# Optimization experiments

Measured on AMD Instinct MI355X. Metric: run time of the kernel, lower is better.

The kernel has to match this reference:

```python
import jax, jax.numpy as jnp
import numpy as np

N = 500          # max_neurons, all alive
INPUT_SIZE = 3072
FEAT_DIM = 64
OUT_SIZE = 10
BATCH = 8192
RADIUS = 20.0
VOL = 100.0      # cubic volume (100,100,100)
N_ITER = 3


def setup_inputs() -> dict:
    key = jax.random.key(0)
    k_x, k_pos, k_iw, k_f, k_ow = jax.random.split(key, 5)
    x = jax.random.normal(k_x, (BATCH, INPUT_SIZE), dtype=jnp.float32)
    # seed positions spread across the volume, roughly matching _init_seeds
    positions = jax.random.uniform(k_pos, (N, 3), dtype=jnp.float32) * 80.0 + 10.0
    input_weights = jax.random.normal(k_iw, (N, INPUT_SIZE), dtype=jnp.float32) * 0.02
    features = jax.random.normal(k_f, (N, FEAT_DIM), dtype=jnp.float32) * 0.1
    output_weights = jax.random.normal(k_ow, (N, OUT_SIZE), dtype=jnp.float32) * 0.02
    biases = jnp.zeros((N,), dtype=jnp.float32)
    return {"x": x, "positions": positions, "input_weights": input_weights,
            "features": features, "output_weights": output_weights, "biases": biases}


def reference(x, positions, input_weights, features, output_weights, biases):
    # clamp positions into the volume (per-axis, vol is cubic here)
    pos = jnp.clip(positions, 0.1, VOL - 0.1)  # [N,3]

    # pairwise distances (grad-safe sqrt at the zero diagonal)
    diff = pos[:, None, :] - pos[None, :, :]          # [N,N,3]
    sq = jnp.sum(diff * diff, axis=-1)                # [N,N]
    pos_mask = sq > 0.0
    dist = jnp.where(pos_mask, jnp.sqrt(jnp.where(pos_mask, sq, 1.0)), 0.0)

    conn_mask = (dist < RADIUS) & (dist > 0.0)
    attenuation = jnp.exp(-dist / RADIUS) * conn_mask.astype(dist.dtype)

    # feature similarity (F.normalize clamps the norm from below at eps)
    feat_norm = features / jnp.maximum(
        jnp.linalg.norm(features, axis=1, keepdims=True), 1e-6)
    feat_sim = jnp.clip(feat_norm @ feat_norm.T, -1.0, 1.0)  # [N,N]

    conn_w = attenuation * (0.5 + 0.5 * feat_sim)
    conn_w = conn_w / (jnp.sum(conn_w, axis=1, keepdims=True) + 1e-6)

    # input gating: neurons near x=0 receive input
    x_norm = pos[:, 0] / VOL                          # [N]
    input_weight = jnp.exp(-2.0 * x_norm)
    input_weight = input_weight / (jnp.sum(input_weight) + 1e-6)

    activations = x @ input_weights.T * input_weight + biases  # [B,N]

    # iterative message passing (fixed small iteration count)
    for _ in range(N_ITER):
        msg = activations @ conn_w.T                  # [B,N]
        activations = jnp.minimum(jax.nn.relu(activations + 0.5 * msg), 50.0)

    # output gating: neurons near x=VOL emit output
    output_weight = jnp.exp(2.0 * (x_norm - 1.0))
    output_weight = output_weight / (jnp.sum(output_weight) + 1e-6)

    return activations @ (output_weights * output_weight[:, None])  # [B,OUT]
```

## Files before the change

### kernel.cpp

```cpp
#include <hip/hip_runtime.h>
#include <stdint.h>

#define N_REAL 500
#define NPAD   512
#define K_IN   3072
#define NBATCH 8192
#define NOUT   10
#define RADIUS 20.0f
#define VOLF   100.0f

typedef __attribute__((ext_vector_type(8))) __bf16 bf16x8;
typedef __attribute__((ext_vector_type(4))) float  f32x4;
typedef __attribute__((ext_vector_type(4))) unsigned short us4;

__device__ __forceinline__ unsigned short f2bf(float f) {
    unsigned int u = __float_as_uint(f);
    u += 0x7FFFu + ((u >> 16) & 1u);
    return (unsigned short)(u >> 16);
}
__device__ __forceinline__ float bf2f(unsigned short h) {
    return __uint_as_float(((unsigned int)h) << 16);
}
__device__ __forceinline__ uint2 cvt_pk4(float4 v) {
    uint2 r;
    asm("v_cvt_pk_bf16_f32 %0, %1, %2" : "=v"(r.x) : "v"(v.x), "v"(v.y));
    asm("v_cvt_pk_bf16_f32 %0, %1, %2" : "=v"(r.y) : "v"(v.z), "v"(v.w));
    return r;
}

#define GLOBAL_AS __attribute__((address_space(1)))
#define LDS_AS    __attribute__((address_space(3)))
__device__ __forceinline__ void glds16(const void* g, void* l) {
    __builtin_amdgcn_global_load_lds((const GLOBAL_AS void*)g, (LDS_AS void*)l, 16, 0, 0);
}

__global__ void prep1(const float* __restrict__ positions,
                      const float* __restrict__ features,
                      const float* __restrict__ out_w,
                      const float* __restrict__ biases,
                      float* __restrict__ feat_norm,
                      float* __restrict__ pos_c,
                      float* __restrict__ inw,
                      float* __restrict__ biasp,
                      float* __restrict__ wout)
{
    int n = threadIdx.x;
    float e_in = 0.f, e_out = 0.f;
    float px = 0.f, py = 0.f, pz = 0.f;
    if (n < N_REAL) {
        px = fminf(fmaxf(positions[n*3+0], 0.1f), VOLF - 0.1f);
        py = fminf(fmaxf(positions[n*3+1], 0.1f), VOLF - 0.1f);
        pz = fminf(fmaxf(positions[n*3+2], 0.1f), VOLF - 0.1f);
        float xn = px / VOLF;
        e_in  = expf(-2.f * xn);
        e_out = expf(2.f * (xn - 1.f));
        float ss = 0.f;
        for (int f = 0; f < 64; ++f) { float v = features[n*64+f]; ss += v*v; }
        float nm = fmaxf(sqrtf(ss), 1e-6f);
        for (int f = 0; f < 64; ++f) feat_norm[n*64+f] = features[n*64+f] / nm;
    } else {
        for (int f = 0; f < 64; ++f) feat_norm[n*64+f] = 0.f;
    }
    pos_c[n*4+0] = px; pos_c[n*4+1] = py; pos_c[n*4+2] = pz; pos_c[n*4+3] = 0.f;

    __shared__ float s_in[512], s_out[512];
    s_in[n] = e_in; s_out[n] = e_out;
    __syncthreads();
    for (int s = 256; s > 0; s >>= 1) {
        if (n < s) { s_in[n] += s_in[n+s]; s_out[n] += s_out[n+s]; }
        __syncthreads();
    }
    float sum_in  = s_in[0]  + 1e-6f;
    float sum_out = s_out[0] + 1e-6f;

    inw[n]   = (n < N_REAL) ? (e_in / sum_in) : 0.f;
    biasp[n] = (n < N_REAL) ? biases[n] : 0.f;
    float wo = (n < N_REAL) ? (e_out / sum_out) : 0.f;
    for (int o = 0; o < NOUT; ++o)
        wout[n*NOUT + o] = (n < N_REAL) ? out_w[n*NOUT + o] * wo : 0.f;
}

__global__ void prep2(const float* __restrict__ pos_c,
                      const float* __restrict__ feat_norm,
                      unsigned short* __restrict__ conn_w)
{
    int i = blockIdx.x;
    int t = threadIdx.x;
    __shared__ float fi[64];
    __shared__ float spos[4];
    __shared__ float red[128];
    if (t < 64) fi[t] = feat_norm[i*64 + t];
    if (t < 4)  spos[t] = pos_c[i*4 + t];
    __syncthreads();

    float w[4];
    float part = 0.f;
    for (int jj = 0; jj < 4; ++jj) {
        int j = t + jj*128;
        float val = 0.f;
        if (i < N_REAL && j < N_REAL) {
            float dx = spos[0] - pos_c[j*4+0];
            float dy = spos[1] - pos_c[j*4+1];
            float dz = spos[2] - pos_c[j*4+2];
            float sq = dx*dx + dy*dy + dz*dz;
            if (sq > 0.f) {
                float dist = sqrtf(sq);
                if (dist < RADIUS) {
                    float att = expf(-dist / RADIUS);
                    float sim = 0.f;
                    const float4* fj = (const float4*)(feat_norm + j*64);
                    const float4* fi4 = (const float4*)fi;
                    #pragma unroll
                    for (int f = 0; f < 16; ++f) {
                        float4 a = fi4[f]; float4 b = fj[f];
                        sim += a.x*b.x + a.y*b.y + a.z*b.z + a.w*b.w;
                    }
                    sim = fminf(fmaxf(sim, -1.f), 1.f);
                    val = att * (0.5f + 0.5f*sim);
                }
            }
        }
        w[jj] = val; part += val;
    }
    red[t] = part;
    __syncthreads();
    for (int s = 64; s > 0; s >>= 1) {
        if (t < s) red[t] += red[t+s];
        __syncthreads();
    }
    float inv = 1.f / (red[0] + 1e-6f);
    for (int jj = 0; jj < 4; ++jj)
        conn_w[(long)i*NPAD + t + jj*128] = f2bf(w[jj] * inv);
}

__global__ void cast_pad(const float* __restrict__ src, unsigned short* __restrict__ dst,
                         long total_q, long src_q)
{
    long i = (long)blockIdx.x * blockDim.x + threadIdx.x;
    long stride = (long)gridDim.x * blockDim.x;
    for (; i < total_q; i += stride) {
        us4 o;
        if (i < src_q) {
            float4 v = ((const float4*)src)[i];
            o[0] = f2bf(v.x); o[1] = f2bf(v.y); o[2] = f2bf(v.z); o[3] = f2bf(v.w);
        } else {
            o[0] = 0; o[1] = 0; o[2] = 0; o[3] = 0;
        }
        ((us4*)dst)[i] = o;
    }
}

__device__ __forceinline__ void block_map(int b, int& m0, int& n0) {
    int xcd = b & 7, loc = b >> 3;
    m0 = (xcd*16 + (loc >> 3)) * 64;
    n0 = (loc & 7) * 64;
}

__global__ __launch_bounds__(256)
void gemm1(const float* __restrict__ X,
           const unsigned short* __restrict__ B,
           unsigned short* __restrict__ Cbf,
           const float* __restrict__ inw,
           const float* __restrict__ biasp)
{
    __shared__ unsigned short As[64*64];
    __shared__ unsigned short Bs[64*64];

    const int tid  = threadIdx.x;
    const int lane = tid & 63;
    const int wave = tid >> 6;
    int m0, n0; block_map(blockIdx.x, m0, n0);
    const int wm = (wave >> 1) * 32;
    const int wn = (wave & 1) * 32;

    f32x4 acc[2][2];
    #pragma unroll
    for (int i = 0; i < 2; ++i)
        #pragma unroll
        for (int j = 0; j < 2; ++j)
            acc[i][j] = (f32x4){0.f,0.f,0.f,0.f};

    const float4* gA[4]; int lAo[4];
    #pragma unroll
    for (int s = 0; s < 4; ++s) {
        int f = tid + s*256;
        int row = f >> 4, c4 = f & 15;
        gA[s] = (const float4*)(X + (long)(m0 + row) * K_IN) + c4;
        lAo[s] = row*128 + ((c4*8) ^ ((row & 7) << 4));
    }
    const char* gB[2]; char* lB[2];
    #pragma unroll
    for (int s = 0; s < 2; ++s) {
        int o = tid*16 + s*4096;
        int row = o >> 7, d = o & 127;
        gB[s] = (const char*)B + (long)(n0 + row) * (K_IN*2) + (d ^ ((row & 7) << 4));
        lB[s] = (char*)Bs + o;
    }

    for (int t = 0; t < 48; ++t) {
        __syncthreads();
        glds16(gB[0], lB[0]);
        glds16(gB[1], lB[1]);
        gB[0] += 128; gB[1] += 128;
        float4 v[4];
        #pragma unroll
        for (int s = 0; s < 4; ++s) { v[s] = gA[s][0]; gA[s] += 16; }
        #pragma unroll
        for (int s = 0; s < 4; ++s)
            *(uint2*)((char*)As + lAo[s]) = cvt_pk4(v[s]);
        asm volatile("s_waitcnt vmcnt(0) lgkmcnt(0)" ::: "memory");
        __syncthreads();

        #pragma unroll
        for (int kk = 0; kk < 2; ++kk) {
            const int cb = kk*64 + (lane >> 4) * 16;
            bf16x8 afr[2], bfr[2];
            #pragma unroll
            for (int i = 0; i < 2; ++i) {
                int r = wm + i*16 + (lane & 15);
                afr[i] = *(const bf16x8*)((const char*)As + r*128 + (cb ^ ((r & 7) << 4)));
            }
            #pragma unroll
            for (int j = 0; j < 2; ++j) {
                int r = wn + j*16 + (lane & 15);
                bfr[j] = *(const bf16x8*)((const char*)Bs + r*128 + (cb ^ ((r & 7) << 4)));
            }
            #pragma unroll
            for (int i = 0; i < 2; ++i)
                #pragma unroll
                for (int j = 0; j < 2; ++j)
                    acc[i][j] = __builtin_amdgcn_mfma_f32_16x16x32_bf16(afr[i], bfr[j], acc[i][j], 0, 0, 0);
        }
    }

    const int mbase = m0 + wm + (lane >> 4) * 4;
    const int nbase = n0 + wn + (lane & 15);
    #pragma unroll
    for (int j = 0; j < 2; ++j) {
        const int n = nbase + j*16;
        const float win = inw[n], bia = biasp[n];
        #pragma unroll
        for (int i = 0; i < 2; ++i)
            #pragma unroll
            for (int r = 0; r < 4; ++r) {
                const long m = mbase + i*16 + r;
                Cbf[m*NPAD + n] = f2bf(acc[i][j][r] * win + bia);
            }
    }
}

__global__ __launch_bounds__(256)
void gemm2(const unsigned short* __restrict__ A,
           const unsigned short* __restrict__ B,
           unsigned short* __restrict__ Cbf,
           const unsigned short* __restrict__ actOld)
{
    __shared__ unsigned short As[64*64];
    __shared__ unsigned short Bs[64*64];

    const int tid  = threadIdx.x;
    const int lane = tid & 63;
    const int wave = tid >> 6;
    int m0, n0; block_map(blockIdx.x, m0, n0);
    const int wm = (wave >> 1) * 32;
    const int wn = (wave & 1) * 32;

    f32x4 acc[2][2];
    #pragma unroll
    for (int i = 0; i < 2; ++i)
        #pragma unroll
        for (int j = 0; j < 2; ++j)
            acc[i][j] = (f32x4){0.f,0.f,0.f,0.f};

    const char* gA[2]; char* lA[2];
    #pragma unroll
    for (int s = 0; s < 2; ++s) {
        int o = tid*16 + s*4096;
        int row = o >> 7, d = o & 127;
        gA[s] = (const char*)A + (long)(m0 + row) * (NPAD*2) + (d ^ ((row & 7) << 4));
        lA[s] = (char*)As + o;
    }
    const char* gB[2]; char* lB[2];
    #pragma unroll
    for (int s = 0; s < 2; ++s) {
        int o = tid*16 + s*4096;
        int row = o >> 7, d = o & 127;
        gB[s] = (const char*)B + (long)(n0 + row) * (NPAD*2) + (d ^ ((row & 7) << 4));
        lB[s] = (char*)Bs + o;
    }

    const int mbase = m0 + wm + (lane >> 4) * 4;
    const int nbase = n0 + wn + (lane & 15);
    unsigned short oldv[2][8];
    #pragma unroll
    for (int j = 0; j < 2; ++j)
        #pragma unroll
        for (int i = 0; i < 2; ++i)
            #pragma unroll
            for (int r = 0; r < 4; ++r)
                oldv[j][i*4+r] = actOld[(long)(mbase + i*16 + r)*NPAD + nbase + j*16];

    for (int t = 0; t < 8; ++t) {
        __syncthreads();
        #pragma unroll
        for (int s = 0; s < 2; ++s) { glds16(gA[s], lA[s]); gA[s] += 128; }
        #pragma unroll
        for (int s = 0; s < 2; ++s) { glds16(gB[s], lB[s]); gB[s] += 128; }
        asm volatile("s_waitcnt vmcnt(0)" ::: "memory");
        __syncthreads();

        #pragma unroll
        for (int kk = 0; kk < 2; ++kk) {
            const int cb = kk*64 + (lane >> 4) * 16;
            bf16x8 afr[2], bfr[2];
            #pragma unroll
            for (int i = 0; i < 2; ++i) {
                int r = wm + i*16 + (lane & 15);
                afr[i] = *(const bf16x8*)((const char*)As + r*128 + (cb ^ ((r & 7) << 4)));
            }
            #pragma unroll
            for (int j = 0; j < 2; ++j) {
                int r = wn + j*16 + (lane & 15);
                bfr[j] = *(const bf16x8*)((const char*)Bs + r*128 + (cb ^ ((r & 7) << 4)));
            }
            #pragma unroll
            for (int i = 0; i < 2; ++i)
                #pragma unroll
                for (int j = 0; j < 2; ++j)
                    acc[i][j] = __builtin_amdgcn_mfma_f32_16x16x32_bf16(afr[i], bfr[j], acc[i][j], 0, 0, 0);
        }
    }

    #pragma unroll
    for (int j = 0; j < 2; ++j) {
        const int n = nbase + j*16;
        #pragma unroll
        for (int i = 0; i < 2; ++i)
            #pragma unroll
            for (int r = 0; r < 4; ++r) {
                const long m = mbase + i*16 + r;
                float old = bf2f(oldv[j][i*4+r]);
                float vv = fminf(fmaxf(old + 0.5f * acc[i][j][r], 0.f), 50.f);
                Cbf[m*NPAD + n] = f2bf(vv);
            }
    }
}

__global__ __launch_bounds__(256)
void out_gemm(const unsigned short* __restrict__ act,
              const float* __restrict__ wout,
              float* __restrict__ out)
{
    __shared__ float sw[NPAD * NOUT];
    const int tid = threadIdx.x;
    for (int i = tid; i < NPAD*NOUT; i += 256) sw[i] = wout[i];
    __syncthreads();

    const int lane = tid & 63;
    const int wv   = tid >> 6;
    const int row  = blockIdx.x * 4 + wv;

    const unsigned short* ap = act + (long)row * NPAD + lane * 8;
    us4 v0 = *(const us4*)(ap);
    us4 v1 = *(const us4*)(ap + 4);

    float p[NOUT];
    #pragma unroll
    for (int o = 0; o < NOUT; ++o) p[o] = 0.f;

    const int nb = lane * 8;
    #pragma unroll
    for (int e = 0; e < 8; ++e) {
        float a = bf2f(e < 4 ? v0[e] : v1[e-4]);
        const float* wr = &sw[(nb + e) * NOUT];
        #pragma unroll
        for (int o = 0; o < NOUT; ++o) p[o] += a * wr[o];
    }
    #pragma unroll
    for (int o = 0; o < NOUT; ++o) {
        float s = p[o];
        for (int d = 32; d > 0; d >>= 1) s += __shfl_down(s, d);
        if (lane == 0) out[(long)row * NOUT + o] = s;
    }
}

extern "C" void kernel_launch(void* const* d_in, const int* in_sizes, int n_in,
                              void* d_out, int out_size, void* d_ws, size_t ws_size,
                              hipStream_t stream)
{
    const float* x        = (const float*)d_in[0];
    const float* pos      = (const float*)d_in[1];
    const float* in_w     = (const float*)d_in[2];
    const float* feats    = (const float*)d_in[3];
    const float* out_w    = (const float*)d_in[4];
    const float* biases   = (const float*)d_in[5];
    float* out = (float*)d_out;

    char* ws = (char*)d_ws;
    unsigned short* iw_bf  = (unsigned short*)(ws);
    unsigned short* connw  = (unsigned short*)(ws + 3145728);
    unsigned short* act_a  = (unsigned short*)(ws + 3670016);
    unsigned short* act_b  = (unsigned short*)(ws + 12058624);
    float* feat_norm = (float*)(ws + 20447232);
    float* pos_c     = (float*)(ws + 20578304);
    float* inw       = (float*)(ws + 20586496);
    float* biasp     = (float*)(ws + 20588544);
    float* wout      = (float*)(ws + 20590592);

    prep1<<<1, 512, 0, stream>>>(pos, feats, out_w, biases, feat_norm, pos_c, inw, biasp, wout);
    prep2<<<512, 128, 0, stream>>>(pos_c, feat_norm, connw);
    cast_pad<<<512, 256, 0, stream>>>(in_w, iw_bf, 393216L, 384000L);

    gemm1<<<1024, 256, 0, stream>>>(x, iw_bf, act_a, inw, biasp);
    gemm2<<<1024, 256, 0, stream>>>(act_a, connw, act_b, act_a);
    gemm2<<<1024, 256, 0, stream>>>(act_b, connw, act_a, act_b);
    gemm2<<<1024, 256, 0, stream>>>(act_a, connw, act_b, act_a);

    out_gemm<<<NBATCH/4, 256, 0, stream>>>(act_b, wout, out);
}
```

Before: 127.2 us.

## Double-buffer LDS tiles in gemm1 and gemm2 to overlap loads with MFMA

```diff
diff --git a/kernel.cpp b/kernel.cpp
--- a/kernel.cpp
+++ b/kernel.cpp
@@ -163,8 +163,8 @@
            const float* __restrict__ inw,
            const float* __restrict__ biasp)
 {
-    __shared__ unsigned short As[64*64];
-    __shared__ unsigned short Bs[64*64];
+    __shared__ unsigned short As[2][64*64];
+    __shared__ unsigned short Bs[2][64*64];
 
     const int tid  = threadIdx.x;
     const int lane = tid & 63;
@@ -188,28 +188,42 @@
         gA[s] = (const float4*)(X + (long)(m0 + row) * K_IN) + c4;
         lAo[s] = row*128 + ((c4*8) ^ ((row & 7) << 4));
     }
-    const char* gB[2]; char* lB[2];
+    const char* gB[2]; int lBo[2];
     #pragma unroll
     for (int s = 0; s < 2; ++s) {
         int o = tid*16 + s*4096;
         int row = o >> 7, d = o & 127;
         gB[s] = (const char*)B + (long)(n0 + row) * (K_IN*2) + (d ^ ((row & 7) << 4));
-        lB[s] = (char*)Bs + o;
-    }
+        lBo[s] = o;
+    }
+
+    float4 v[4];
+    #pragma unroll
+    for (int s = 0; s < 4; ++s) { v[s] = gA[s][0]; gA[s] += 16; }
+    __builtin_amdgcn_sched_barrier(0);
+    glds16(gB[0], (char*)Bs[0] + lBo[0]);
+    glds16(gB[1], (char*)Bs[0] + lBo[1]);
+    gB[0] += 128; gB[1] += 128;
+    #pragma unroll
+    for (int s = 0; s < 4; ++s)
+        *(uint2*)((char*)As[0] + lAo[s]) = cvt_pk4(v[s]);
+    asm volatile("s_waitcnt lgkmcnt(0)" ::: "memory");
 
     for (int t = 0; t < 48; ++t) {
-        __syncthreads();
-        glds16(gB[0], lB[0]);
-        glds16(gB[1], lB[1]);
-        gB[0] += 128; gB[1] += 128;
-        float4 v[4];
-        #pragma unroll
-        for (int s = 0; s < 4; ++s) { v[s] = gA[s][0]; gA[s] += 16; }
-        #pragma unroll
-        for (int s = 0; s < 4; ++s)
-            *(uint2*)((char*)As + lAo[s]) = cvt_pk4(v[s]);
-        asm volatile("s_waitcnt vmcnt(0) lgkmcnt(0)" ::: "memory");
-        __syncthreads();
+        const int cur = t & 1;
+        const bool more = (t < 47);
+        if (more) {
+            #pragma unroll
+            for (int s = 0; s < 4; ++s) { v[s] = gA[s][0]; gA[s] += 16; }
+            __builtin_amdgcn_sched_barrier(0);
+            glds16(gB[0], (char*)Bs[cur^1] + lBo[0]);
+            glds16(gB[1], (char*)Bs[cur^1] + lBo[1]);
+            gB[0] += 128; gB[1] += 128;
+            asm volatile("s_waitcnt vmcnt(6)" ::: "memory");
+        } else {
+            asm volatile("s_waitcnt vmcnt(0)" ::: "memory");
+        }
+        __builtin_amdgcn_s_barrier();
 
         #pragma unroll
         for (int kk = 0; kk < 2; ++kk) {
@@ -218,18 +232,26 @@
             #pragma unroll
             for (int i = 0; i < 2; ++i) {
                 int r = wm + i*16 + (lane & 15);
-                afr[i] = *(const bf16x8*)((const char*)As + r*128 + (cb ^ ((r & 7) << 4)));
+                afr[i] = *(const bf16x8*)((const char*)As[cur] + r*128 + (cb ^ ((r & 7) << 4)));
             }
             #pragma unroll
             for (int j = 0; j < 2; ++j) {
                 int r = wn + j*16 + (lane & 15);
-                bfr[j] = *(const bf16x8*)((const char*)Bs + r*128 + (cb ^ ((r & 7) << 4)));
+                bfr[j] = *(const bf16x8*)((const char*)Bs[cur] + r*128 + (cb ^ ((r & 7) << 4)));
             }
             #pragma unroll
             for (int i = 0; i < 2; ++i)
                 #pragma unroll
                 for (int j = 0; j < 2; ++j)
                     acc[i][j] = __builtin_amdgcn_mfma_f32_16x16x32_bf16(afr[i], bfr[j], acc[i][j], 0, 0, 0);
+        }
+
+        if (more) {
+            #pragma unroll
+            for (int s = 0; s < 4; ++s)
+                *(uint2*)((char*)As[cur^1] + lAo[s]) = cvt_pk4(v[s]);
+            asm volatile("s_waitcnt lgkmcnt(0)" ::: "memory");
+            __builtin_amdgcn_s_barrier();
         }
     }
 
@@ -255,8 +277,8 @@
            unsigned short* __restrict__ Cbf,
            const unsigned short* __restrict__ actOld)
 {
-    __shared__ unsigned short As[64*64];
-    __shared__ unsigned short Bs[64*64];
+    __shared__ unsigned short As[2][64*64];
+    __shared__ unsigned short Bs[2][64*64];
 
     const int tid  = threadIdx.x;
     const int lane = tid & 63;
@@ -272,42 +294,41 @@
         for (int j = 0; j < 2; ++j)
             acc[i][j] = (f32x4){0.f,0.f,0.f,0.f};
 
-    const char* gA[2]; char* lA[2];
+    const char* gA[2]; int lAo[2];
     #pragma unroll
     for (int s = 0; s < 2; ++s) {
         int o = tid*16 + s*4096;
         int row = o >> 7, d = o & 127;
         gA[s] = (const char*)A + (long)(m0 + row) * (NPAD*2) + (d ^ ((row & 7) << 4));
-        lA[s] = (char*)As + o;
-    }
-    const char* gB[2]; char* lB[2];
+        lAo[s] = o;
+    }
+    const char* gB[2]; int lBo[2];
     #pragma unroll
     for (int s = 0; s < 2; ++s) {
         int o = tid*16 + s*4096;
         int row = o >> 7, d = o & 127;
         gB[s] = (const char*)B + (long)(n0 + row) * (NPAD*2) + (d ^ ((row & 7) << 4));
-        lB[s] = (char*)Bs + o;
-    }
-
-    const int mbase = m0 + wm + (lane >> 4) * 4;
-    const int nbase = n0 + wn + (lane & 15);
-    unsigned short oldv[2][8];
-    #pragma unroll
-    for (int j = 0; j < 2; ++j)
-        #pragma unroll
-        for (int i = 0; i < 2; ++i)
-            #pragma unroll
-            for (int r = 0; r < 4; ++r)
-                oldv[j][i*4+r] = actOld[(long)(mbase + i*16 + r)*NPAD + nbase + j*16];
+        lBo[s] = o;
+    }
+
+    #pragma unroll
+    for (int s = 0; s < 2; ++s) { glds16(gA[s], (char*)As[0] + lAo[s]); gA[s] += 128; }
+    #pragma unroll
+    for (int s = 0; s < 2; ++s) { glds16(gB[s], (char*)Bs[0] + lBo[s]); gB[s] += 128; }
 
     for (int t = 0; t < 8; ++t) {
-        __syncthreads();
-        #pragma unroll
-        for (int s = 0; s < 2; ++s) { glds16(gA[s], lA[s]); gA[s] += 128; }
-        #pragma unroll
-        for (int s = 0; s < 2; ++s) { glds16(gB[s], lB[s]); gB[s] += 128; }
-        asm volatile("s_waitcnt vmcnt(0)" ::: "memory");
-        __syncthreads();
+        const int cur = t & 1;
+        const bool more = (t < 7);
+        if (more) {
+            #pragma unroll
+            for (int s = 0; s < 2; ++s) { glds16(gA[s], (char*)As[cur^1] + lAo[s]); gA[s] += 128; }
+            #pragma unroll
+            for (int s = 0; s < 2; ++s) { glds16(gB[s], (char*)Bs[cur^1] + lBo[s]); gB[s] += 128; }
+            asm volatile("s_waitcnt vmcnt(4)" ::: "memory");
+        } else {
+            asm volatile("s_waitcnt vmcnt(0)" ::: "memory");
+        }
+        __builtin_amdgcn_s_barrier();
 
         #pragma unroll
         for (int kk = 0; kk < 2; ++kk) {
@@ -316,12 +337,12 @@
             #pragma unroll
             for (int i = 0; i < 2; ++i) {
                 int r = wm + i*16 + (lane & 15);
-                afr[i] = *(const bf16x8*)((const char*)As + r*128 + (cb ^ ((r & 7) << 4)));
+                afr[i] = *(const bf16x8*)((const char*)As[cur] + r*128 + (cb ^ ((r & 7) << 4)));
             }
             #pragma unroll
             for (int j = 0; j < 2; ++j) {
                 int r = wn + j*16 + (lane & 15);
-                bfr[j] = *(const bf16x8*)((const char*)Bs + r*128 + (cb ^ ((r & 7) << 4)));
+                bfr[j] = *(const bf16x8*)((const char*)Bs[cur] + r*128 + (cb ^ ((r & 7) << 4)));
             }
             #pragma unroll
             for (int i = 0; i < 2; ++i)
@@ -329,8 +350,13 @@
                 for (int j = 0; j < 2; ++j)
                     acc[i][j] = __builtin_amdgcn_mfma_f32_16x16x32_bf16(afr[i], bfr[j], acc[i][j], 0, 0, 0);
         }
-    }
-
+
+        if (more)
+            __builtin_amdgcn_s_barrier();
+    }
+
+    const int mbase = m0 + wm + (lane >> 4) * 4;
+    const int nbase = n0 + wn + (lane & 15);
     #pragma unroll
     for (int j = 0; j < 2; ++j) {
         const int n = nbase + j*16;
@@ -339,7 +365,7 @@
             #pragma unroll
             for (int r = 0; r < 4; ++r) {
                 const long m = mbase + i*16 + r;
-                float old = bf2f(oldv[j][i*4+r]);
+                float old = bf2f(actOld[m*NPAD + n]);
                 float vv = fminf(fmaxf(old + 0.5f * acc[i][j][r], 0.f), 50.f);
                 Cbf[m*NPAD + n] = f2bf(vv);
             }
```

Result: slower. 130.8 us (+2.8%).

## Split-K the input GEMM and triple-buffer the message-passing GEMM with wider tiles

Applied to the files above, without the earlier changes.

```diff
diff --git a/kernel.cpp b/kernel.cpp
--- a/kernel.cpp
+++ b/kernel.cpp
@@ -150,18 +150,21 @@
     }
 }
 
-__device__ __forceinline__ void block_map(int b, int& m0, int& n0) {
+__device__ __forceinline__ void block_map_g1(int b, int& m0, int& n0) {
     int xcd = b & 7, loc = b >> 3;
     m0 = (xcd*16 + (loc >> 3)) * 64;
     n0 = (loc & 7) * 64;
 }
+__device__ __forceinline__ void block_map_g2(int b, int& m0, int& n0) {
+    int xcd = b & 7, loc = b >> 3;
+    m0 = (xcd*16 + (loc >> 2)) * 64;
+    n0 = (loc & 3) * 128;
+}
 
 __global__ __launch_bounds__(256)
-void gemm1(const float* __restrict__ X,
-           const unsigned short* __restrict__ B,
-           unsigned short* __restrict__ Cbf,
-           const float* __restrict__ inw,
-           const float* __restrict__ biasp)
+void gemm1s(const float* __restrict__ X,
+            const unsigned short* __restrict__ B,
+            float* __restrict__ Pf)
 {
     __shared__ unsigned short As[64*64];
     __shared__ unsigned short Bs[64*64];
@@ -169,7 +172,10 @@
     const int tid  = threadIdx.x;
     const int lane = tid & 63;
     const int wave = tid >> 6;
-    int m0, n0; block_map(blockIdx.x, m0, n0);
+    const int bs   = blockIdx.x & 1023;
+    const int ks   = blockIdx.x >> 10;
+    const int kbase = ks * (K_IN/2);
+    int m0, n0; block_map_g1(bs, m0, n0);
     const int wm = (wave >> 1) * 32;
     const int wn = (wave & 1) * 32;
 
@@ -185,7 +191,7 @@
     for (int s = 0; s < 4; ++s) {
         int f = tid + s*256;
         int row = f >> 4, c4 = f & 15;
-        gA[s] = (const float4*)(X + (long)(m0 + row) * K_IN) + c4;
+        gA[s] = (const float4*)(X + (long)(m0 + row) * K_IN + kbase) + c4;
         lAo[s] = row*128 + ((c4*8) ^ ((row & 7) << 4));
     }
     const char* gB[2]; char* lB[2];
@@ -193,11 +199,11 @@
     for (int s = 0; s < 2; ++s) {
         int o = tid*16 + s*4096;
         int row = o >> 7, d = o & 127;
-        gB[s] = (const char*)B + (long)(n0 + row) * (K_IN*2) + (d ^ ((row & 7) << 4));
+        gB[s] = (const char*)B + (long)(n0 + row) * (K_IN*2) + kbase*2 + (d ^ ((row & 7) << 4));
         lB[s] = (char*)Bs + o;
     }
 
-    for (int t = 0; t < 48; ++t) {
+    for (int t = 0; t < 24; ++t) {
         __syncthreads();
         glds16(gB[0], lB[0]);
         glds16(gB[1], lB[1]);
@@ -233,113 +239,155 @@
         }
     }
 
+    float* P = Pf + (long)ks * (NBATCH * (long)NPAD);
     const int mbase = m0 + wm + (lane >> 4) * 4;
     const int nbase = n0 + wn + (lane & 15);
     #pragma unroll
     for (int j = 0; j < 2; ++j) {
         const int n = nbase + j*16;
-        const float win = inw[n], bia = biasp[n];
         #pragma unroll
         for (int i = 0; i < 2; ++i)
             #pragma unroll
             for (int r = 0; r < 4; ++r) {
                 const long m = mbase + i*16 + r;
-                Cbf[m*NPAD + n] = f2bf(acc[i][j][r] * win + bia);
+                P[m*NPAD + n] = acc[i][j][r];
             }
     }
 }
 
 __global__ __launch_bounds__(256)
-void gemm2(const unsigned short* __restrict__ A,
-           const unsigned short* __restrict__ B,
-           unsigned short* __restrict__ Cbf,
-           const unsigned short* __restrict__ actOld)
-{
-    __shared__ unsigned short As[64*64];
-    __shared__ unsigned short Bs[64*64];
+void reduce_ep(const float* __restrict__ Pf,
+               const float* __restrict__ inw,
+               const float* __restrict__ biasp,
+               unsigned short* __restrict__ act)
+{
+    const long TOTQ = (long)NBATCH * NPAD / 4;
+    long i = (long)blockIdx.x * blockDim.x + threadIdx.x;
+    long stride = (long)gridDim.x * blockDim.x;
+    for (; i < TOTQ; i += stride) {
+        float4 a = ((const float4*)Pf)[i];
+        float4 b = ((const float4*)Pf)[i + TOTQ];
+        int nq = (int)(i & 127);
+        float4 w  = ((const float4*)inw)[nq];
+        float4 bi = ((const float4*)biasp)[nq];
+        us4 o;
+        o[0] = f2bf((a.x + b.x) * w.x + bi.x);
+        o[1] = f2bf((a.y + b.y) * w.y + bi.y);
+        o[2] = f2bf((a.z + b.z) * w.z + bi.z);
+        o[3] = f2bf((a.w + b.w) * w.w + bi.w);
+        ((us4*)act)[i] = o;
+    }
+}
+
+__global__ __launch_bounds__(256, 4)
+void gemm2_pipe(const unsigned short* __restrict__ A,
+                const unsigned short* __restrict__ B,
+                unsigned short* __restrict__ Cbf,
+                const unsigned short* __restrict__ actOld)
+{
+    constexpr int ABUF = 8192;
+    constexpr int BBUF = 16384;
+    __shared__ __align__(16) char lds[3*(ABUF+BBUF)];
+    char* const Abase = lds;
+    char* const Bbase = lds + 3*ABUF;
 
     const int tid  = threadIdx.x;
     const int lane = tid & 63;
     const int wave = tid >> 6;
-    int m0, n0; block_map(blockIdx.x, m0, n0);
+    int m0, n0; block_map_g2(blockIdx.x, m0, n0);
     const int wm = (wave >> 1) * 32;
-    const int wn = (wave & 1) * 32;
-
-    f32x4 acc[2][2];
+    const int wn = (wave & 1) * 64;
+
+    f32x4 acc[2][4];
     #pragma unroll
     for (int i = 0; i < 2; ++i)
         #pragma unroll
-        for (int j = 0; j < 2; ++j)
+        for (int j = 0; j < 4; ++j)
             acc[i][j] = (f32x4){0.f,0.f,0.f,0.f};
 
-    const char* gA[2]; char* lA[2];
+    const char* gB[4]; int lBo[4];
+    #pragma unroll
+    for (int s = 0; s < 4; ++s) {
+        int o = tid*16 + s*4096;
+        int row = o >> 7, d = o & 127;
+        gB[s] = (const char*)B + (long)(n0 + row) * (NPAD*2) + (d ^ ((row & 7) << 4));
+        lBo[s] = o;
+    }
+    const char* gA1[2]; int lAo1[2];
     #pragma unroll
     for (int s = 0; s < 2; ++s) {
         int o = tid*16 + s*4096;
         int row = o >> 7, d = o & 127;
-        gA[s] = (const char*)A + (long)(m0 + row) * (NPAD*2) + (d ^ ((row & 7) << 4));
-        lA[s] = (char*)As + o;
-    }
-    const char* gB[2]; char* lB[2];
-    #pragma unroll
-    for (int s = 0; s < 2; ++s) {
-        int o = tid*16 + s*4096;
-        int row = o >> 7, d = o & 127;
-        gB[s] = (const char*)B + (long)(n0 + row) * (NPAD*2) + (d ^ ((row & 7) << 4));
-        lB[s] = (char*)Bs + o;
+        gA1[s] = (const char*)A + (long)(m0 + row) * (NPAD*2) + (d ^ ((row & 7) << 4));
+        lAo1[s] = o;
+    }
+
+    const int NT = NPAD >> 6;
+
+    #pragma unroll
+    for (int s = 0; s < 2; ++s) { glds16(gA1[s], Abase + 0*ABUF + lAo1[s]); gA1[s] += 128; }
+    #pragma unroll
+    for (int s = 0; s < 4; ++s) { glds16(gB[s], Bbase + 0*BBUF + lBo[s]); gB[s] += 128; }
+    #pragma unroll
+    for (int s = 0; s < 2; ++s) { glds16(gA1[s], Abase + 1*ABUF + lAo1[s]); gA1[s] += 128; }
+    #pragma unroll
+    for (int s = 0; s < 4; ++s) { glds16(gB[s], Bbase + 1*BBUF + lBo[s]); gB[s] += 128; }
+
+    int cur = 0;
+    for (int t = 0; t < NT; ++t) {
+        int fb = cur + 2; if (fb >= 3) fb -= 3;
+        const bool more2 = (t + 2 < NT);
+        const bool more1 = (t + 1 < NT);
+        if (more2) {
+            #pragma unroll
+            for (int s = 0; s < 2; ++s) { glds16(gA1[s], Abase + fb*ABUF + lAo1[s]); gA1[s] += 128; }
+            #pragma unroll
+            for (int s = 0; s < 4; ++s) { glds16(gB[s], Bbase + fb*BBUF + lBo[s]); gB[s] += 128; }
+            asm volatile("s_waitcnt vmcnt(12)" ::: "memory");
+        } else if (more1) {
+            asm volatile("s_waitcnt vmcnt(6)" ::: "memory");
+        } else {
+            asm volatile("s_waitcnt vmcnt(0)" ::: "memory");
+        }
+        __builtin_amdgcn_s_barrier();
+
+        const char* Ab = Abase + cur*ABUF;
+        const char* Bb = Bbase + cur*BBUF;
+        #pragma unroll
+        for (int kk = 0; kk < 2; ++kk) {
+            const int cb = kk*64 + (lane >> 4) * 16;
+            bf16x8 afr[2], bfr[4];
+            #pragma unroll
+            for (int i = 0; i < 2; ++i) {
+                int r = wm + i*16 + (lane & 15);
+                afr[i] = *(const bf16x8*)(Ab + r*128 + (cb ^ ((r & 7) << 4)));
+            }
+            #pragma unroll
+            for (int j = 0; j < 4; ++j) {
+                int r = wn + j*16 + (lane & 15);
+                bfr[j] = *(const bf16x8*)(Bb + r*128 + (cb ^ ((r & 7) << 4)));
+            }
+            #pragma unroll
+            for (int i = 0; i < 2; ++i)
+                #pragma unroll
+                for (int j = 0; j < 4; ++j)
+                    acc[i][j] = __builtin_amdgcn_mfma_f32_16x16x32_bf16(afr[i], bfr[j], acc[i][j], 0, 0, 0);
+        }
+        __builtin_amdgcn_s_barrier();
+        cur = (cur == 2) ? 0 : cur + 1;
     }
 
     const int mbase = m0 + wm + (lane >> 4) * 4;
     const int nbase = n0 + wn + (lane & 15);
-    unsigned short oldv[2][8];
-    #pragma unroll
-    for (int j = 0; j < 2; ++j)
-        #pragma unroll
-        for (int i = 0; i < 2; ++i)
-            #pragma unroll
-            for (int r = 0; r < 4; ++r)
-                oldv[j][i*4+r] = actOld[(long)(mbase + i*16 + r)*NPAD + nbase + j*16];
-
-    for (int t = 0; t < 8; ++t) {
-        __syncthreads();
-        #pragma unroll
-        for (int s = 0; s < 2; ++s) { glds16(gA[s], lA[s]); gA[s] += 128; }
-        #pragma unroll
-        for (int s = 0; s < 2; ++s) { glds16(gB[s], lB[s]); gB[s] += 128; }
-        asm volatile("s_waitcnt vmcnt(0)" ::: "memory");
-        __syncthreads();
-
-        #pragma unroll
-        for (int kk = 0; kk < 2; ++kk) {
-            const int cb = kk*64 + (lane >> 4) * 16;
-            bf16x8 afr[2], bfr[2];
-            #pragma unroll
-            for (int i = 0; i < 2; ++i) {
-                int r = wm + i*16 + (lane & 15);
-                afr[i] = *(const bf16x8*)((const char*)As + r*128 + (cb ^ ((r & 7) << 4)));
-            }
-            #pragma unroll
-            for (int j = 0; j < 2; ++j) {
-                int r = wn + j*16 + (lane & 15);
-                bfr[j] = *(const bf16x8*)((const char*)Bs + r*128 + (cb ^ ((r & 7) << 4)));
-            }
-            #pragma unroll
-            for (int i = 0; i < 2; ++i)
-                #pragma unroll
-                for (int j = 0; j < 2; ++j)
-                    acc[i][j] = __builtin_amdgcn_mfma_f32_16x16x32_bf16(afr[i], bfr[j], acc[i][j], 0, 0, 0);
-        }
-    }
-
-    #pragma unroll
-    for (int j = 0; j < 2; ++j) {
+    #pragma unroll
+    for (int j = 0; j < 4; ++j) {
         const int n = nbase + j*16;
         #pragma unroll
         for (int i = 0; i < 2; ++i)
             #pragma unroll
             for (int r = 0; r < 4; ++r) {
                 const long m = mbase + i*16 + r;
-                float old = bf2f(oldv[j][i*4+r]);
+                float old = bf2f(actOld[m*NPAD + n]);
                 float vv = fminf(fmaxf(old + 0.5f * acc[i][j][r], 0.f), 50.f);
                 Cbf[m*NPAD + n] = f2bf(vv);
             }
@@ -406,15 +454,18 @@
     float* inw       = (float*)(ws + 20586496);
     float* biasp     = (float*)(ws + 20588544);
     float* wout      = (float*)(ws + 20590592);
+    float* partials  = (float*)(ws + 20611072);
 
     prep1<<<1, 512, 0, stream>>>(pos, feats, out_w, biases, feat_norm, pos_c, inw, biasp, wout);
     prep2<<<512, 128, 0, stream>>>(pos_c, feat_norm, connw);
     cast_pad<<<512, 256, 0, stream>>>(in_w, iw_bf, 393216L, 384000L);
 
-    gemm1<<<1024, 256, 0, stream>>>(x, iw_bf, act_a, inw, biasp);
-    gemm2<<<1024, 256, 0, stream>>>(act_a, connw, act_b, act_a);
-    gemm2<<<1024, 256, 0, stream>>>(act_b, connw, act_a, act_b);
-    gemm2<<<1024, 256, 0, stream>>>(act_a, connw, act_b, act_a);
+    gemm1s<<<2048, 256, 0, stream>>>(x, iw_bf, partials);
+    reduce_ep<<<2048, 256, 0, stream>>>(partials, inw, biasp, act_a);
+
+    gemm2_pipe<<<512, 256, 0, stream>>>(act_a, connw, act_b, act_a);
+    gemm2_pipe<<<512, 256, 0, stream>>>(act_b, connw, act_a, act_b);
+    gemm2_pipe<<<512, 256, 0, stream>>>(act_a, connw, act_b, act_a);
 
     out_gemm<<<NBATCH/4, 256, 0, stream>>>(act_b, wout, out);
 }
```

New measurement: 131.7 us. 1.03x slower.
